# Kernel optimization log

Hardware: AMD Instinct MI355X
Metric: run time of the kernel (lower is better)

The kernel has to match this reference:

```python
import jax, jax.numpy as jnp
import numpy as np

TEMPERATURE = 0.07
EPS = 1e-12  # F.normalize eps


def setup_inputs() -> dict:
    key = jax.random.key(0)
    k1, k2 = jax.random.split(key)
    B, D = 4096, 1024
    return {
        "features_1": jax.random.normal(k1, (B, D), dtype=jnp.float32),
        "features_2": jax.random.normal(k2, (B, D), dtype=jnp.float32),
    }


def _l2_normalize(x):
    n = jnp.sqrt(jnp.sum(x * x, axis=1, keepdims=True))
    return x / jnp.maximum(n, EPS)


def reference(features_1, features_2):
    B = features_1.shape[0]
    f1 = _l2_normalize(features_1)
    f2 = _l2_normalize(features_2)
    f = jnp.concatenate([f1, f2], axis=0)  # [2B, D]
    # cosine sim of already-normalized vectors == plain matmul
    sim = (f @ f.T) / TEMPERATURE  # [2B, 2B]
    # denominator: logsumexp over each row excluding the diagonal (self-sim)
    eye = jnp.eye(2 * B, dtype=bool)
    lse = jax.nn.logsumexp(jnp.where(eye, -jnp.inf, sim), axis=1)  # [2B]
    # positives: cross-view pairs (i+B, i) then (i, i+B)
    idx = jnp.arange(B)
    pos = jnp.concatenate([sim[idx + B, idx], sim[idx, idx + B]], axis=0)  # [2B]
    loss = -jnp.mean(pos - lse)
    return loss
```

## Files before the change

### kernel.cpp

```cpp
#include <hip/hip_runtime.h>
#include <hip/hip_bf16.h>
#include <math.h>

#define INV_T (1.0f / 0.07f)

typedef __bf16 bf16x8 __attribute__((ext_vector_type(8)));
typedef float f32x4 __attribute__((ext_vector_type(4)));

__device__ __forceinline__ void gld16(const void* g, void* l) {
    __builtin_amdgcn_global_load_lds(
        (const __attribute__((address_space(1))) unsigned int*)g,
        (__attribute__((address_space(3))) unsigned int*)l,
        16, 0, 0);
}

__device__ __forceinline__ float agent_load(const float* p) {
    return __hip_atomic_load(p, __ATOMIC_RELAXED, __HIP_MEMORY_SCOPE_AGENT);
}

__global__ __launch_bounds__(256) void norm_kernel(
    const float4* __restrict__ f1, const float4* __restrict__ f2,
    ushort4* __restrict__ F, float* __restrict__ S, float* __restrict__ P,
    int* __restrict__ cnt, int B) {
    const int i = blockIdx.x;
    const int t = threadIdx.x;

    float4 x = f1[i * 256 + t];
    float4 y = f2[i * 256 + t];

    float s1 = x.x * x.x + x.y * x.y + x.z * x.z + x.w * x.w;
    float s2 = y.x * y.x + y.y * y.y + y.z * y.z + y.w * y.w;
    float dd = x.x * y.x + x.y * y.y + x.z * y.z + x.w * y.w;

    for (int o = 32; o > 0; o >>= 1) {
        s1 += __shfl_down(s1, o);
        s2 += __shfl_down(s2, o);
        dd += __shfl_down(dd, o);
    }
    __shared__ float red[4][3];
    const int wv = t >> 6, ln = t & 63;
    if (ln == 0) { red[wv][0] = s1; red[wv][1] = s2; red[wv][2] = dd; }
    __syncthreads();
    s1 = red[0][0] + red[1][0] + red[2][0] + red[3][0];
    s2 = red[0][1] + red[1][1] + red[2][1] + red[3][1];
    dd = red[0][2] + red[1][2] + red[2][2] + red[3][2];

    const float rn1 = 1.0f / fmaxf(sqrtf(s1), 1e-12f);
    const float rn2 = 1.0f / fmaxf(sqrtf(s2), 1e-12f);

    union { ushort4 u; __hip_bfloat16 h[4]; } p;
    p.h[0] = __float2bfloat16(x.x * rn1);
    p.h[1] = __float2bfloat16(x.y * rn1);
    p.h[2] = __float2bfloat16(x.z * rn1);
    p.h[3] = __float2bfloat16(x.w * rn1);
    F[(size_t)i * 256 + t] = p.u;
    p.h[0] = __float2bfloat16(y.x * rn2);
    p.h[1] = __float2bfloat16(y.y * rn2);
    p.h[2] = __float2bfloat16(y.z * rn2);
    p.h[3] = __float2bfloat16(y.w * rn2);
    F[(size_t)(B + i) * 256 + t] = p.u;

    if (t == 0) {
        P[i] = dd * rn1 * rn2;
        S[i] = 0.0f;
        S[B + i] = 0.0f;
        if (i == 0) *cnt = 0;
    }
}

__global__ __launch_bounds__(256, 2) void sim_kernel(
    const __hip_bfloat16* __restrict__ F, float* __restrict__ S,
    const float* __restrict__ P, float* __restrict__ out,
    int* __restrict__ cnt, int N, int B, int D) {
    __shared__ __align__(16) __hip_bfloat16 As[128][64];
    __shared__ __align__(16) __hip_bfloat16 Bs[256][64];

    const int k = blockIdx.x;
    int tj = (int)((sqrtf(4.0f * (float)k + 1.0f) - 1.0f) * 0.5f);
    while ((tj + 1) * (tj + 2) <= k) ++tj;
    while (tj * (tj + 1) > k) --tj;
    const int ti = k - tj * (tj + 1);
    const int bRow = ti * 128;
    const int bCol = tj * 256;

    const int tid  = threadIdx.x;
    const int wave = tid >> 6;
    const int lane = tid & 63;
    const int quad = lane >> 4;
    const int l16  = lane & 15;

    const int srow   = lane >> 3;
    const int ldsOff = (lane & 7) * 8;
    const int srcOff = ((lane & 7) ^ srow) * 8;

    const int waveRow = (wave >> 1) * 64;
    const int waveCol = (wave & 1) * 128;
    const int swz = l16 & 7;

    f32x4 acc[4][8];
#pragma unroll
    for (int mi = 0; mi < 4; ++mi)
#pragma unroll
        for (int ni = 0; ni < 8; ++ni)
            acc[mi][ni] = (f32x4){0.0f, 0.0f, 0.0f, 0.0f};

    for (int kb = 0; kb < D; kb += 64) {
#pragma unroll
        for (int p = 0; p < 4; ++p) {
            const int rowT = (p * 4 + wave) * 8 + srow;
            gld16(&F[(size_t)(bRow + rowT) * D + kb + srcOff], &As[rowT][ldsOff]);
        }
#pragma unroll
        for (int p = 0; p < 8; ++p) {
            const int rowT = (p * 4 + wave) * 8 + srow;
            gld16(&F[(size_t)(bCol + rowT) * D + kb + srcOff], &Bs[rowT][ldsOff]);
        }
        __syncthreads();

#pragma unroll
        for (int ks = 0; ks < 2; ++ks) {
            const int slot = ((ks * 4 + quad) ^ swz) * 8;
            bf16x8 bf[8];
#pragma unroll
            for (int ni = 0; ni < 8; ++ni)
                bf[ni] = *(const bf16x8*)&Bs[waveCol + ni * 16 + l16][slot];
#pragma unroll
            for (int mi = 0; mi < 4; ++mi) {
                const bf16x8 af = *(const bf16x8*)&As[waveRow + mi * 16 + l16][slot];
#pragma unroll
                for (int ni = 0; ni < 8; ++ni)
                    acc[mi][ni] = __builtin_amdgcn_mfma_f32_16x16x32_bf16(
                        af, bf[ni], acc[mi][ni], 0, 0, 0);
            }
        }
        __syncthreads();
    }

#pragma unroll
    for (int mi = 0; mi < 4; ++mi)
#pragma unroll
        for (int ni = 0; ni < 8; ++ni)
#pragma unroll
            for (int r = 0; r < 4; ++r) {
                const int gRow = bRow + waveRow + mi * 16 + quad * 4 + r;
                const int gCol = bCol + waveCol + ni * 16 + l16;
                acc[mi][ni][r] = (gRow < gCol)
                    ? __expf((acc[mi][ni][r] - 1.0f) * INV_T) : 0.0f;
            }

#pragma unroll
    for (int mi = 0; mi < 4; ++mi)
#pragma unroll
        for (int r = 0; r < 4; ++r) {
            const int gRow = bRow + waveRow + mi * 16 + quad * 4 + r;
            float v = 0.0f;
#pragma unroll
            for (int ni = 0; ni < 8; ++ni) v += acc[mi][ni][r];
            v += __shfl_xor(v, 1);
            v += __shfl_xor(v, 2);
            v += __shfl_xor(v, 4);
            v += __shfl_xor(v, 8);
            if (l16 == 0) atomicAdd(&S[gRow], v);
        }

#pragma unroll
    for (int ni = 0; ni < 8; ++ni) {
        float cv = 0.0f;
#pragma unroll
        for (int mi = 0; mi < 4; ++mi)
#pragma unroll
            for (int r = 0; r < 4; ++r) cv += acc[mi][ni][r];
        cv += __shfl_xor(cv, 16);
        cv += __shfl_xor(cv, 32);
        if (quad == 0) atomicAdd(&S[bCol + waveCol + ni * 16 + l16], cv);
    }

    asm volatile("s_waitcnt vmcnt(0) lgkmcnt(0)" ::: "memory");
    __shared__ int lastFlag;
    if (tid == 0) lastFlag = (atomicAdd(cnt, 1) == (int)gridDim.x - 1);
    __syncthreads();
    if (!lastFlag) return;

    float s0 = 0.0f, s1 = 0.0f, s2 = 0.0f, s3 = 0.0f;
    for (int i = tid; i < N; i += 1024) {
        const float a = agent_load(&S[i]);
        const float b = agent_load(&S[i + 256]);
        const float c = agent_load(&S[i + 512]);
        const float d = agent_load(&S[i + 768]);
        s0 += __logf(a); s1 += __logf(b); s2 += __logf(c); s3 += __logf(d);
    }
    float s = (s0 + s1) + (s2 + s3);

    float pp = 0.0f;
    for (int i = tid; i < B; i += 1024)
        pp += P[i] + P[i + 256] + P[i + 512] + P[i + 768];

    for (int o = 32; o > 0; o >>= 1) {
        s += __shfl_down(s, o);
        pp += __shfl_down(pp, o);
    }
    __shared__ float redf[4][2];
    if (lane == 0) { redf[wave][0] = s; redf[wave][1] = pp; }
    __syncthreads();
    if (tid == 0) {
        const float sl = redf[0][0] + redf[1][0] + redf[2][0] + redf[3][0];
        const float ps = redf[0][1] + redf[1][1] + redf[2][1] + redf[3][1];
        out[0] = INV_T + sl / (float)N - ps * (2.0f * INV_T / (float)N);
    }
}

extern "C" void kernel_launch(void* const* d_in, const int* in_sizes, int n_in,
                              void* d_out, int out_size, void* d_ws, size_t ws_size,
                              hipStream_t stream) {
    const int D = 1024;
    const int B = in_sizes[0] / D;
    const int N = 2 * B;
    const int M2 = N / 256;
    const int ntiles = M2 * M2 + M2;

    const float* f1 = (const float*)d_in[0];
    const float* f2 = (const float*)d_in[1];

    __hip_bfloat16* F = (__hip_bfloat16*)d_ws;
    float* S = (float*)((char*)d_ws + (size_t)N * D * sizeof(__hip_bfloat16));
    float* P = S + N;
    int* cnt = (int*)(P + B);

    norm_kernel<<<dim3(B), dim3(256), 0, stream>>>(
        (const float4*)f1, (const float4*)f2, (ushort4*)F, S, P, cnt, B);
    sim_kernel<<<dim3(ntiles), dim3(256), 0, stream>>>(
        F, S, P, (float*)d_out, cnt, N, B, D);
}
```

Measured before the change: 171.2 us.

## Use persistent blocks with atomic work queue over smaller 128x128 triangular tiles

The similarity kernel now launches a fixed grid of 1024 persistent blocks that pull tile indices from an atomic counter. Tiles shrink from 128x256 rectangles to 128x128 squares enumerated over the upper triangle, which cuts wasted compute on the diagonal and balances load across CUs. In exchange, each tile reuses less data from the loaded panels, and the per-tile atomic fetch and extra barrier add overhead. A second counter handles last-block detection for the final reduction.

```diff
diff --git a/kernel.cpp b/kernel.cpp
--- a/kernel.cpp
+++ b/kernel.cpp
@@ -64,24 +64,17 @@
         P[i] = dd * rn1 * rn2;
         S[i] = 0.0f;
         S[B + i] = 0.0f;
-        if (i == 0) *cnt = 0;
+        if (i == 0) { cnt[0] = 0; cnt[1] = 0; }
     }
 }
 
 __global__ __launch_bounds__(256, 2) void sim_kernel(
     const __hip_bfloat16* __restrict__ F, float* __restrict__ S,
     const float* __restrict__ P, float* __restrict__ out,
-    int* __restrict__ cnt, int N, int B, int D) {
+    int* __restrict__ cnt, int N, int B, int D, int ntiles) {
     __shared__ __align__(16) __hip_bfloat16 As[128][64];
-    __shared__ __align__(16) __hip_bfloat16 Bs[256][64];
-
-    const int k = blockIdx.x;
-    int tj = (int)((sqrtf(4.0f * (float)k + 1.0f) - 1.0f) * 0.5f);
-    while ((tj + 1) * (tj + 2) <= k) ++tj;
-    while (tj * (tj + 1) > k) --tj;
-    const int ti = k - tj * (tj + 1);
-    const int bRow = ti * 128;
-    const int bCol = tj * 256;
+    __shared__ __align__(16) __hip_bfloat16 Bs[128][64];
+    __shared__ int kShared;
 
     const int tid  = threadIdx.x;
     const int wave = tid >> 6;
@@ -94,90 +87,102 @@
     const int srcOff = ((lane & 7) ^ srow) * 8;
 
     const int waveRow = (wave >> 1) * 64;
-    const int waveCol = (wave & 1) * 128;
+    const int waveCol = (wave & 1) * 64;
     const int swz = l16 & 7;
 
-    f32x4 acc[4][8];
-#pragma unroll
-    for (int mi = 0; mi < 4; ++mi)
-#pragma unroll
-        for (int ni = 0; ni < 8; ++ni)
-            acc[mi][ni] = (f32x4){0.0f, 0.0f, 0.0f, 0.0f};
-
-    for (int kb = 0; kb < D; kb += 64) {
-#pragma unroll
-        for (int p = 0; p < 4; ++p) {
-            const int rowT = (p * 4 + wave) * 8 + srow;
-            gld16(&F[(size_t)(bRow + rowT) * D + kb + srcOff], &As[rowT][ldsOff]);
+    for (;;) {
+        if (tid == 0) kShared = atomicAdd(&cnt[0], 1);
+        __syncthreads();
+        const int k = kShared;
+        if (k >= ntiles) break;
+
+        int tjj = (int)((sqrtf(8.0f * (float)k + 1.0f) - 1.0f) * 0.5f);
+        while ((tjj + 1) * (tjj + 2) / 2 <= k) ++tjj;
+        while (tjj * (tjj + 1) / 2 > k) --tjj;
+        const int tii = k - tjj * (tjj + 1) / 2;
+        const int bRow = tii * 128;
+        const int bCol = tjj * 128;
+
+        f32x4 acc[4][4];
+#pragma unroll
+        for (int mi = 0; mi < 4; ++mi)
+#pragma unroll
+            for (int ni = 0; ni < 4; ++ni)
+                acc[mi][ni] = (f32x4){0.0f, 0.0f, 0.0f, 0.0f};
+
+        for (int kb = 0; kb < D; kb += 64) {
+#pragma unroll
+            for (int p = 0; p < 4; ++p) {
+                const int rowT = (p * 4 + wave) * 8 + srow;
+                gld16(&F[(size_t)(bRow + rowT) * D + kb + srcOff], &As[rowT][ldsOff]);
+            }
+#pragma unroll
+            for (int p = 0; p < 4; ++p) {
+                const int rowT = (p * 4 + wave) * 8 + srow;
+                gld16(&F[(size_t)(bCol + rowT) * D + kb + srcOff], &Bs[rowT][ldsOff]);
+            }
+            __syncthreads();
+
+#pragma unroll
+            for (int ks = 0; ks < 2; ++ks) {
+                const int slot = ((ks * 4 + quad) ^ swz) * 8;
+                bf16x8 bf[4];
+#pragma unroll
+                for (int ni = 0; ni < 4; ++ni)
+                    bf[ni] = *(const bf16x8*)&Bs[waveCol + ni * 16 + l16][slot];
+#pragma unroll
+                for (int mi = 0; mi < 4; ++mi) {
+                    const bf16x8 af = *(const bf16x8*)&As[waveRow + mi * 16 + l16][slot];
+#pragma unroll
+                    for (int ni = 0; ni < 4; ++ni)
+                        acc[mi][ni] = __builtin_amdgcn_mfma_f32_16x16x32_bf16(
+                            af, bf[ni], acc[mi][ni], 0, 0, 0);
+                }
+            }
+            __syncthreads();
         }
-#pragma unroll
-        for (int p = 0; p < 8; ++p) {
-            const int rowT = (p * 4 + wave) * 8 + srow;
-            gld16(&F[(size_t)(bCol + rowT) * D + kb + srcOff], &Bs[rowT][ldsOff]);
-        }
-        __syncthreads();
-
-#pragma unroll
-        for (int ks = 0; ks < 2; ++ks) {
-            const int slot = ((ks * 4 + quad) ^ swz) * 8;
-            bf16x8 bf[8];
-#pragma unroll
-            for (int ni = 0; ni < 8; ++ni)
-                bf[ni] = *(const bf16x8*)&Bs[waveCol + ni * 16 + l16][slot];
-#pragma unroll
-            for (int mi = 0; mi < 4; ++mi) {
-                const bf16x8 af = *(const bf16x8*)&As[waveRow + mi * 16 + l16][slot];
-#pragma unroll
-                for (int ni = 0; ni < 8; ++ni)
-                    acc[mi][ni] = __builtin_amdgcn_mfma_f32_16x16x32_bf16(
-                        af, bf[ni], acc[mi][ni], 0, 0, 0);
-            }
-        }
-        __syncthreads();
-    }
-
-#pragma unroll
-    for (int mi = 0; mi < 4; ++mi)
-#pragma unroll
-        for (int ni = 0; ni < 8; ++ni)
+
+#pragma unroll
+        for (int mi = 0; mi < 4; ++mi)
+#pragma unroll
+            for (int ni = 0; ni < 4; ++ni)
+#pragma unroll
+                for (int r = 0; r < 4; ++r) {
+                    const int gRow = bRow + waveRow + mi * 16 + quad * 4 + r;
+                    const int gCol = bCol + waveCol + ni * 16 + l16;
+                    acc[mi][ni][r] = (gRow < gCol)
+                        ? __expf((acc[mi][ni][r] - 1.0f) * INV_T) : 0.0f;
+                }
+
+#pragma unroll
+        for (int mi = 0; mi < 4; ++mi)
 #pragma unroll
             for (int r = 0; r < 4; ++r) {
                 const int gRow = bRow + waveRow + mi * 16 + quad * 4 + r;
-                const int gCol = bCol + waveCol + ni * 16 + l16;
-                acc[mi][ni][r] = (gRow < gCol)
-                    ? __expf((acc[mi][ni][r] - 1.0f) * INV_T) : 0.0f;
-            }
-
-#pragma unroll
-    for (int mi = 0; mi < 4; ++mi)
-#pragma unroll
-        for (int r = 0; r < 4; ++r) {
-            const int gRow = bRow + waveRow + mi * 16 + quad * 4 + r;
-            float v = 0.0f;
-#pragma unroll
-            for (int ni = 0; ni < 8; ++ni) v += acc[mi][ni][r];
-            v += __shfl_xor(v, 1);
-            v += __shfl_xor(v, 2);
-            v += __shfl_xor(v, 4);
-            v += __shfl_xor(v, 8);
-            if (l16 == 0) atomicAdd(&S[gRow], v);
+                float v = acc[mi][0][r] + acc[mi][1][r] + acc[mi][2][r] + acc[mi][3][r];
+                v += __shfl_xor(v, 1);
+                v += __shfl_xor(v, 2);
+                v += __shfl_xor(v, 4);
+                v += __shfl_xor(v, 8);
+                if (l16 == 0) atomicAdd(&S[gRow], v);
+            }
+
+#pragma unroll
+        for (int ni = 0; ni < 4; ++ni) {
+            float cv = 0.0f;
+#pragma unroll
+            for (int mi = 0; mi < 4; ++mi)
+#pragma unroll
+                for (int r = 0; r < 4; ++r) cv += acc[mi][ni][r];
+            cv += __shfl_xor(cv, 16);
+            cv += __shfl_xor(cv, 32);
+            if (quad == 0) atomicAdd(&S[bCol + waveCol + ni * 16 + l16], cv);
         }
-
-#pragma unroll
-    for (int ni = 0; ni < 8; ++ni) {
-        float cv = 0.0f;
-#pragma unroll
-        for (int mi = 0; mi < 4; ++mi)
-#pragma unroll
-            for (int r = 0; r < 4; ++r) cv += acc[mi][ni][r];
-        cv += __shfl_xor(cv, 16);
-        cv += __shfl_xor(cv, 32);
-        if (quad == 0) atomicAdd(&S[bCol + waveCol + ni * 16 + l16], cv);
     }
 
     asm volatile("s_waitcnt vmcnt(0) lgkmcnt(0)" ::: "memory");
     __shared__ int lastFlag;
-    if (tid == 0) lastFlag = (atomicAdd(cnt, 1) == (int)gridDim.x - 1);
+    if (tid == 0) lastFlag = (atomicAdd(&cnt[1], 1) == (int)gridDim.x - 1);
     __syncthreads();
     if (!lastFlag) return;
 
@@ -215,8 +220,9 @@
     const int D = 1024;
     const int B = in_sizes[0] / D;
     const int N = 2 * B;
-    const int M2 = N / 256;
-    const int ntiles = M2 * M2 + M2;
+    const int M = N / 128;
+    const int ntiles = M * (M + 1) / 2;
+    const int nblocks = 1024;
 
     const float* f1 = (const float*)d_in[0];
     const float* f2 = (const float*)d_in[1];
@@ -228,6 +234,6 @@
 
     norm_kernel<<<dim3(B), dim3(256), 0, stream>>>(
         (const float4*)f1, (const float4*)f2, (ushort4*)F, S, P, cnt, B);
-    sim_kernel<<<dim3(ntiles), dim3(256), 0, stream>>>(
-        F, S, P, (float*)d_out, cnt, N, B, D);
-}
+    sim_kernel<<<dim3(nblocks), dim3(256), 0, stream>>>(
+        F, S, P, (float*)d_out, cnt, N, B, D, ntiles);
+}
```

After: 174.0 us. About the same (+1.6%).
